# Optimization experiments

Hardware: AMD Instinct MI355X
Metric: run time of the kernel (lower is better)

The kernel has to match this reference:

```python
import jax, jax.numpy as jnp
import numpy as np

L2_LAMDA = 0.001
RECONS_LAMDA = 0.2
LB_TH = 0.01
B, N, D = 32, 2048, 256


def setup_inputs() -> dict:
    key = jax.random.key(0)
    k1, k2, k3, k4 = jax.random.split(key, 4)
    cur = jax.random.normal(k1, (B, N, D), jnp.float32)
    pre = jax.random.normal(k2, (B, N, D), jnp.float32)
    lim_r = float(np.sqrt(6.0 / (D + D)))  # xavier_uniform bound
    r_proj = jax.random.uniform(k3, (D, D), jnp.float32, -lim_r, lim_r)
    lim_i = float(np.sqrt(6.0 / (N + N)))
    incidence_m = jax.random.uniform(k4, (N, N), jnp.float32, -lim_i, lim_i)
    return {"cur": cur, "pre": pre, "r_proj": r_proj, "incidence_m": incidence_m}


def reference(cur, pre, r_proj, incidence_m):
    # torch forward detaches cur/pre
    cur = jax.lax.stop_gradient(cur)
    pre = jax.lax.stop_gradient(pre)
    # clamp(min=lb_th) then zero where not (> lb_th)  ==  keep original where > lb_th else 0
    W = jnp.where(incidence_m > LB_TH, incidence_m, 0.0)          # (N, N)
    proj = jnp.einsum('bnd,de->bne', cur, r_proj)                 # (B, N, D)
    neigh = jnp.einsum('nm,bmd->bnd', W, pre)                     # (B, N, D)
    recon_err = jnp.sqrt(jnp.sum((proj - neigh) ** 2, axis=-1))   # (B, N)
    # torch: max(sum(abs(row[None,:]), dim=0)) == max-abs of the masked row
    l1 = jnp.max(jnp.abs(W), axis=1)                              # (N,)
    l2 = jnp.sqrt(jnp.sum(W ** 2, axis=1))                        # (N,)
    per_node = recon_err * RECONS_LAMDA + l1[None, :] + L2_LAMDA * l2[None, :]
    loss = jnp.sum(per_node, axis=1, keepdims=True)               # (B, 1)
    return loss, incidence_m
```

## Files before the change

### kernel.cpp

```cpp
#include <hip/hip_runtime.h>


typedef __attribute__((ext_vector_type(8))) short bf16x8;
typedef __attribute__((ext_vector_type(8))) unsigned short ushort8;
typedef __attribute__((ext_vector_type(16))) float f32x16;

__device__ __forceinline__ unsigned short f2bf(float f) {
    union { float f; unsigned u; } x; x.f = f;
    unsigned r = x.u + 0x7fffu + ((x.u >> 16) & 1u);
    return (unsigned short)(r >> 16);
}

#define GLL16(g, l)                                                         \
    __builtin_amdgcn_global_load_lds(                                       \
        (const __attribute__((address_space(1))) void*)(g),                 \
        (__attribute__((address_space(3))) void*)(l), 16, 0, 0)

__device__ __forceinline__ void transpose_64x64(
    const float* __restrict__ src, unsigned short* __restrict__ dst,
    int R, int C, int r0, int c0, unsigned short* __restrict__ tile) {
    const int t = threadIdx.x;
    const int fr = t >> 4, fc = (t & 15) * 4;
#pragma unroll
    for (int it = 0; it < 4; ++it) {
        int m = fr + it * 16;
        float4 v = *(const float4*)(src + (size_t)(r0 + m) * C + c0 + fc);
        tile[(fc + 0) * 68 + m] = f2bf(v.x);
        tile[(fc + 1) * 68 + m] = f2bf(v.y);
        tile[(fc + 2) * 68 + m] = f2bf(v.z);
        tile[(fc + 3) * 68 + m] = f2bf(v.w);
    }
    __syncthreads();
    const int d = t >> 2, m0 = (t & 3) * 16;
    unsigned short v[16];
#pragma unroll
    for (int j = 0; j < 4; ++j)
        *(ushort4*)(v + j * 4) = *(const ushort4*)(tile + d * 68 + m0 + j * 4);
    unsigned short* dp = dst + (size_t)(c0 + d) * R + r0 + m0;
    ushort8 p0, p1;
#pragma unroll
    for (int j = 0; j < 8; ++j) { p0[j] = v[j]; p1[j] = v[8 + j]; }
    *(ushort8*)(dp) = p0;
    *(ushort8*)(dp + 8) = p1;
}

__global__ __launch_bounds__(256) void prep_all(
    const float* __restrict__ inc, float* __restrict__ out_inc,
    unsigned short* __restrict__ Wneg, float* __restrict__ crow,
    const float* __restrict__ pre, unsigned short* __restrict__ preT,
    const float* __restrict__ r_proj, unsigned short* __restrict__ rprojT,
    const float* __restrict__ cur, unsigned short* __restrict__ curbf,
    float* __restrict__ out_loss) {
    __shared__ unsigned short tile[64 * 68];
    __shared__ float smax[4], ssum[4];
    const int bid = blockIdx.x;
    const int t = threadIdx.x;

    if (bid < 2048) {
        if (bid == 0 && t < 32) out_loss[t] = 0.f;
        const int row = bid;
        const float4* src = (const float4*)(inc + (size_t)row * 2048);
        float4* dst = (float4*)(out_inc + (size_t)row * 2048);
        ushort4* wp = (ushort4*)(Wneg + (size_t)row * 2048);
        float lmax = 0.f, ss = 0.f;
#pragma unroll
        for (int it = 0; it < 2; ++it) {
            int i = it * 256 + t;
            float4 v = src[i];
            dst[i] = v;
            float w0 = v.x > 0.01f ? v.x : 0.f;
            float w1 = v.y > 0.01f ? v.y : 0.f;
            float w2 = v.z > 0.01f ? v.z : 0.f;
            float w3 = v.w > 0.01f ? v.w : 0.f;
            ushort4 p;
            p.x = f2bf(-w0); p.y = f2bf(-w1); p.z = f2bf(-w2); p.w = f2bf(-w3);
            wp[i] = p;
            lmax = fmaxf(lmax, fmaxf(fmaxf(w0, w1), fmaxf(w2, w3)));
            ss += w0 * w0 + w1 * w1 + w2 * w2 + w3 * w3;
        }
#pragma unroll
        for (int off = 32; off; off >>= 1) {
            lmax = fmaxf(lmax, __shfl_down(lmax, off));
            ss += __shfl_down(ss, off);
        }
        int wv = t >> 6, ln = t & 63;
        if (ln == 0) { smax[wv] = lmax; ssum[wv] = ss; }
        __syncthreads();
        if (t == 0) {
            float m = fmaxf(fmaxf(smax[0], smax[1]), fmaxf(smax[2], smax[3]));
            float s = ssum[0] + ssum[1] + ssum[2] + ssum[3];
            crow[row] = m + 0.001f * sqrtf(s);
        }
    } else if (bid < 6144) {
        const int tt = bid - 2048;
        const int b = tt >> 7;
        const int mt = (tt & 127) >> 2;
        const int dt = tt & 3;
        transpose_64x64(pre + (size_t)b * 524288, preT + (size_t)b * 524288,
                        2048, 256, mt * 64, dt * 64, tile);
    } else if (bid < 6160) {
        const int tt = bid - 6144;
        transpose_64x64(r_proj, rprojT, 256, 256, (tt >> 2) * 64, (tt & 3) * 64,
                        tile);
    } else {
        const size_t base = (size_t)(bid - 6160) * 8192;
#pragma unroll
        for (int i = 0; i < 8; ++i) {
            size_t idx = base + (size_t)(i * 256 + t) * 4;
            float4 v = *(const float4*)(cur + idx);
            ushort4 p;
            p.x = f2bf(v.x); p.y = f2bf(v.y); p.z = f2bf(v.z); p.w = f2bf(v.w);
            *(ushort4*)(curbf + idx) = p;
        }
    }
}

__global__ __launch_bounds__(1024) void gemm_diff(
    const unsigned short* __restrict__ Wneg,
    const unsigned short* __restrict__ curbf,
    const unsigned short* __restrict__ preT,
    const unsigned short* __restrict__ rprojT,
    const float* __restrict__ crow,
    float* __restrict__ out_loss)
{
    const int i    = blockIdx.x;
    const int xcd  = i & 7;
    const int slot = i >> 3;
    const int n0   = (slot & 7) * 256;
    const int b    = xcd + ((slot >> 3) << 3);

    __shared__ unsigned short Ab[4 * 256 * 32];
    __shared__ unsigned short Bb[4 * 256 * 32];
    __shared__ float ssq[256];
    __shared__ float red[16];

    const int tid  = threadIdx.x;
    const int w    = tid >> 6;
    const int lane = tid & 63;
    const int l32  = lane & 31;
    const int half = lane >> 5;
    const int wm   = w >> 2;
    const int wn   = w & 3;
    const int w16  = w * 16;
    const int srow  = lane >> 2;
    const int sbyte = ((lane & 3) ^ ((lane >> 3) & 3)) * 16;
    const int q2    = (l32 >> 1) & 3;

    if (tid < 256) ssq[tid] = 0.f;

    f32x16 acc[2][2] = {};

    const unsigned short* curA = curbf + (size_t)b * 2048 * 256 + (size_t)n0 * 256;
    const unsigned short* preB = preT + (size_t)b * 256 * 2048;
    const unsigned short* An   = Wneg + (size_t)n0 * 2048;

#define STAGEPAIR(T, AB, AS, BB, BS, KK)                                       \
    {                                                                          \
        GLL16((const char*)((AB) + (size_t)(w16 + srow) * (AS) + (KK)) + sbyte,\
              (char*)Ab + ((T) & 3) * 16384 + w * 1024);                       \
        GLL16((const char*)((BB) + (size_t)(w16 + srow) * (BS) + (KK)) + sbyte,\
              (char*)Bb + ((T) & 3) * 16384 + w * 1024);                       \
    }

    STAGEPAIR(0, An, 2048, preB, 2048, 0);
    STAGEPAIR(1, An, 2048, preB, 2048, 32);
    STAGEPAIR(2, An, 2048, preB, 2048, 64);

    for (int t = 0; t < 72; ++t) {
        if (t < 70)       asm volatile("s_waitcnt vmcnt(4)" ::: "memory");
        else if (t == 70) asm volatile("s_waitcnt vmcnt(2)" ::: "memory");
        else              asm volatile("s_waitcnt vmcnt(0)" ::: "memory");
        asm volatile("s_barrier" ::: "memory");

        if (t < 69) {
            const int t3 = t + 3;
            const unsigned short *aB, *bB;
            int aS, bS, kk;
            if (t3 < 64) { aB = An;   aS = 2048; bB = preB;   bS = 2048; kk = t3 * 32; }
            else         { aB = curA; aS = 256;  bB = rprojT; bS = 256;  kk = (t3 - 64) * 32; }
            STAGEPAIR(t3, aB, aS, bB, bS, kk);
        }

        const unsigned short* Ac = Ab + (t & 3) * 8192;
        const unsigned short* Bc = Bb + (t & 3) * 8192;
#pragma unroll
        for (int ks = 0; ks < 2; ++ks) {
            const int co = (((ks << 1) + half) ^ q2) << 3;
            bf16x8 af[2], bfr[2];
#pragma unroll
            for (int mi = 0; mi < 2; ++mi)
                af[mi] = *(const bf16x8*)(Ac + (wm * 64 + mi * 32 + l32) * 32 + co);
#pragma unroll
            for (int ni = 0; ni < 2; ++ni)
                bfr[ni] = *(const bf16x8*)(Bc + (wn * 64 + ni * 32 + l32) * 32 + co);
#pragma unroll
            for (int mi = 0; mi < 2; ++mi)
#pragma unroll
                for (int ni = 0; ni < 2; ++ni)
                    acc[mi][ni] = __builtin_amdgcn_mfma_f32_32x32x16_bf16(
                        af[mi], bfr[ni], acc[mi][ni], 0, 0, 0);
        }
    }
    __syncthreads();

#pragma unroll
    for (int mi = 0; mi < 2; ++mi)
#pragma unroll
        for (int reg = 0; reg < 16; ++reg) {
            float s = 0.f;
#pragma unroll
            for (int ni = 0; ni < 2; ++ni) {
                float v = acc[mi][ni][reg];
                s += v * v;
            }
            s += __shfl_xor(s, 1);
            s += __shfl_xor(s, 2);
            s += __shfl_xor(s, 4);
            s += __shfl_xor(s, 8);
            s += __shfl_xor(s, 16);
            if (l32 == 0) {
                const int row = wm * 64 + mi * 32 +
                                (reg & 3) + 8 * (reg >> 2) + 4 * half;
                atomicAdd(&ssq[row], s);
            }
        }
    __syncthreads();

    float contrib = 0.f;
    if (tid < 256) contrib = 0.2f * sqrtf(ssq[tid]) + crow[n0 + tid];
#pragma unroll
    for (int off = 32; off; off >>= 1) contrib += __shfl_down(contrib, off);
    if (lane == 0) red[w] = contrib;
    __syncthreads();
    if (tid == 0) {
        float s = 0.f;
#pragma unroll
        for (int k = 0; k < 16; ++k) s += red[k];
        atomicAdd(out_loss + b, s);
    }
}

extern "C" void kernel_launch(void* const* d_in, const int* in_sizes, int n_in,
                              void* d_out, int out_size, void* d_ws, size_t ws_size,
                              hipStream_t stream) {
    const float* cur    = (const float*)d_in[0];
    const float* pre    = (const float*)d_in[1];
    const float* r_proj = (const float*)d_in[2];
    const float* inc    = (const float*)d_in[3];
    float* out = (float*)d_out;

    char* ws = (char*)d_ws;
    unsigned short* Wneg   = (unsigned short*)(ws + 0);
    unsigned short* preT   = (unsigned short*)(ws + 8388608);
    unsigned short* rprojT = (unsigned short*)(ws + 41943040);
    float*          crow   = (float*)(ws + 42336256);
    unsigned short* curbf  = (unsigned short*)(ws + 42344448);

    prep_all<<<8208, 256, 0, stream>>>(inc, out + 32, Wneg, crow,
                                       pre, preT, r_proj, rprojT,
                                       cur, curbf, out);
    gemm_diff<<<256, 1024, 0, stream>>>(Wneg, curbf, preT, rprojT, crow, out);
}
```

Baseline: 258.2 us.

## Shrink GEMM tile to 128 rows with 512 threads and triple buffering

Halves the M tile of the fused GEMM (128 rows instead of 256) and the block size (512 threads), doubling the grid to 512 blocks. The LDS pipeline goes from 4 stages with prefetch distance 3 to 3 stages with distance 2. Each block now loads the B tile in two halves. The aim is more blocks per CU and better occupancy across the 256 CUs, at the cost of loading the pre/rproj B tiles twice as often and a shallower prefetch.

Result: no change. 259.3 us (+0.4%).

```diff
diff --git a/kernel.cpp b/kernel.cpp
--- a/kernel.cpp
+++ b/kernel.cpp
@@ -115,7 +115,7 @@
     }
 }
 
-__global__ __launch_bounds__(1024) void gemm_diff(
+__global__ __launch_bounds__(512) void gemm_diff(
     const unsigned short* __restrict__ Wneg,
     const unsigned short* __restrict__ curbf,
     const unsigned short* __restrict__ preT,
@@ -126,13 +126,13 @@
     const int i    = blockIdx.x;
     const int xcd  = i & 7;
     const int slot = i >> 3;
-    const int n0   = (slot & 7) * 256;
-    const int b    = xcd + ((slot >> 3) << 3);
-
-    __shared__ unsigned short Ab[4 * 256 * 32];
-    __shared__ unsigned short Bb[4 * 256 * 32];
-    __shared__ float ssq[256];
-    __shared__ float red[16];
+    const int n0   = (slot & 15) * 128;
+    const int b    = xcd + ((slot >> 4) << 3);
+
+    __shared__ unsigned short Ab[3 * 128 * 32];
+    __shared__ unsigned short Bb[3 * 256 * 32];
+    __shared__ float ssq[128];
+    __shared__ float red[8];
 
     const int tid  = threadIdx.x;
     const int w    = tid >> 6;
@@ -146,7 +146,7 @@
     const int sbyte = ((lane & 3) ^ ((lane >> 3) & 3)) * 16;
     const int q2    = (l32 >> 1) & 3;
 
-    if (tid < 256) ssq[tid] = 0.f;
+    if (tid < 128) ssq[tid] = 0.f;
 
     f32x16 acc[2][2] = {};
 
@@ -154,35 +154,34 @@
     const unsigned short* preB = preT + (size_t)b * 256 * 2048;
     const unsigned short* An   = Wneg + (size_t)n0 * 2048;
 
-#define STAGEPAIR(T, AB, AS, BB, BS, KK)                                       \
+#define STAGE(BUF, aB, aS, bB, bS, KK)                                         \
     {                                                                          \
-        GLL16((const char*)((AB) + (size_t)(w16 + srow) * (AS) + (KK)) + sbyte,\
-              (char*)Ab + ((T) & 3) * 16384 + w * 1024);                       \
-        GLL16((const char*)((BB) + (size_t)(w16 + srow) * (BS) + (KK)) + sbyte,\
-              (char*)Bb + ((T) & 3) * 16384 + w * 1024);                       \
-    }
-
-    STAGEPAIR(0, An, 2048, preB, 2048, 0);
-    STAGEPAIR(1, An, 2048, preB, 2048, 32);
-    STAGEPAIR(2, An, 2048, preB, 2048, 64);
-
+        GLL16((const char*)((aB) + (size_t)(w16 + srow) * (aS) + (KK)) + sbyte,\
+              (char*)Ab + (BUF) * 8192 + w16 * 64);                            \
+        GLL16((const char*)((bB) + (size_t)(w16 + srow) * (bS) + (KK)) + sbyte,\
+              (char*)Bb + (BUF) * 16384 + w16 * 64);                           \
+        GLL16((const char*)((bB) + (size_t)(128 + w16 + srow) * (bS) + (KK)) + sbyte,\
+              (char*)Bb + (BUF) * 16384 + (128 + w16) * 64);                   \
+    }
+
+    STAGE(0, An, 2048, preB, 2048, 0);
+    STAGE(1, An, 2048, preB, 2048, 32);
+
+    int bc = 0;
     for (int t = 0; t < 72; ++t) {
-        if (t < 70)       asm volatile("s_waitcnt vmcnt(4)" ::: "memory");
-        else if (t == 70) asm volatile("s_waitcnt vmcnt(2)" ::: "memory");
-        else              asm volatile("s_waitcnt vmcnt(0)" ::: "memory");
+        if (t < 71) asm volatile("s_waitcnt vmcnt(3)" ::: "memory");
+        else        asm volatile("s_waitcnt vmcnt(0)" ::: "memory");
         asm volatile("s_barrier" ::: "memory");
 
-        if (t < 69) {
-            const int t3 = t + 3;
-            const unsigned short *aB, *bB;
-            int aS, bS, kk;
-            if (t3 < 64) { aB = An;   aS = 2048; bB = preB;   bS = 2048; kk = t3 * 32; }
-            else         { aB = curA; aS = 256;  bB = rprojT; bS = 256;  kk = (t3 - 64) * 32; }
-            STAGEPAIR(t3, aB, aS, bB, bS, kk);
-        }
-
-        const unsigned short* Ac = Ab + (t & 3) * 8192;
-        const unsigned short* Bc = Bb + (t & 3) * 8192;
+        if (t < 70) {
+            const int t2 = t + 2;
+            const int bs = bc >= 1 ? bc - 1 : bc + 2;
+            if (t2 < 64) { STAGE(bs, An,   2048, preB,   2048, t2 * 32); }
+            else         { STAGE(bs, curA, 256,  rprojT, 256,  (t2 - 64) * 32); }
+        }
+
+        const unsigned short* Ac = Ab + bc * 4096;
+        const unsigned short* Bc = Bb + bc * 8192;
 #pragma unroll
         for (int ks = 0; ks < 2; ++ks) {
             const int co = (((ks << 1) + half) ^ q2) << 3;
@@ -200,6 +199,7 @@
                     acc[mi][ni] = __builtin_amdgcn_mfma_f32_32x32x16_bf16(
                         af[mi], bfr[ni], acc[mi][ni], 0, 0, 0);
         }
+        bc = bc < 2 ? bc + 1 : 0;
     }
     __syncthreads();
 
@@ -227,7 +227,7 @@
     __syncthreads();
 
     float contrib = 0.f;
-    if (tid < 256) contrib = 0.2f * sqrtf(ssq[tid]) + crow[n0 + tid];
+    if (tid < 128) contrib = 0.2f * sqrtf(ssq[tid]) + crow[n0 + tid];
 #pragma unroll
     for (int off = 32; off; off >>= 1) contrib += __shfl_down(contrib, off);
     if (lane == 0) red[w] = contrib;
@@ -235,7 +235,7 @@
     if (tid == 0) {
         float s = 0.f;
 #pragma unroll
-        for (int k = 0; k < 16; ++k) s += red[k];
+        for (int k = 0; k < 8; ++k) s += red[k];
         atomicAdd(out_loss + b, s);
     }
 }
@@ -259,5 +259,5 @@
     prep_all<<<8208, 256, 0, stream>>>(inc, out + 32, Wneg, crow,
                                        pre, preT, r_proj, rprojT,
                                        cur, curbf, out);
-    gemm_diff<<<256, 1024, 0, stream>>>(Wneg, curbf, preT, rprojT, crow, out);
-}
+    gemm_diff<<<512, 512, 0, stream>>>(Wneg, curbf, preT, rprojT, crow, out);
+}
```

## Restructure GEMM into 8-wave 128x64 warp tiles with 16x16x32 MFMA and ping-pong phases

Applied to the files above, without the earlier changes.

Drops the GEMM block from 16 to 8 waves, giving each wave a 128x64 output tile built from 16x16x32 bf16 MFMAs. The K-step grows to 64 with double-buffered LDS in place of the 4-deep ring. The main loop is split into barrier-separated phases that interleave global-to-LDS loads with MFMA bursts under raised s_setprio, and B fragments are reused across two A halves. The aim is more register-level reuse and fewer LDS reads and barriers per FLOP, at the cost of higher register pressure and a tighter load/compute schedule.

After: 242.7 us. -6.0%, faster.

```diff
diff --git a/kernel.cpp b/kernel.cpp
--- a/kernel.cpp
+++ b/kernel.cpp
@@ -3,7 +3,7 @@
 
 typedef __attribute__((ext_vector_type(8))) short bf16x8;
 typedef __attribute__((ext_vector_type(8))) unsigned short ushort8;
-typedef __attribute__((ext_vector_type(16))) float f32x16;
+typedef __attribute__((ext_vector_type(4))) float f32x4;
 
 __device__ __forceinline__ unsigned short f2bf(float f) {
     union { float f; unsigned u; } x; x.f = f;
@@ -115,7 +115,7 @@
     }
 }
 
-__global__ __launch_bounds__(1024) void gemm_diff(
+__global__ __launch_bounds__(512) void gemm_diff(
     const unsigned short* __restrict__ Wneg,
     const unsigned short* __restrict__ curbf,
     const unsigned short* __restrict__ preT,
@@ -129,98 +129,125 @@
     const int n0   = (slot & 7) * 256;
     const int b    = xcd + ((slot >> 3) << 3);
 
-    __shared__ unsigned short Ab[4 * 256 * 32];
-    __shared__ unsigned short Bb[4 * 256 * 32];
+    __shared__ unsigned short Ab[2 * 256 * 64];
+    __shared__ unsigned short Bb[2 * 256 * 64];
     __shared__ float ssq[256];
-    __shared__ float red[16];
+    __shared__ float red[8];
 
     const int tid  = threadIdx.x;
     const int w    = tid >> 6;
     const int lane = tid & 63;
-    const int l32  = lane & 31;
-    const int half = lane >> 5;
+    const int l15  = lane & 15;
+    const int kg   = lane >> 4;
     const int wm   = w >> 2;
     const int wn   = w & 3;
-    const int w16  = w * 16;
-    const int srow  = lane >> 2;
-    const int sbyte = ((lane & 3) ^ ((lane >> 3) & 3)) * 16;
-    const int q2    = (l32 >> 1) & 3;
+    const int srow  = lane >> 3;
+    const int sbyte = ((lane & 7) ^ srow) * 16;
+    const int rsw   = (lane & 7) << 4;
+    const int csw0 = (kg * 16) ^ rsw;
+    const int csw1 = (64 + kg * 16) ^ rsw;
 
     if (tid < 256) ssq[tid] = 0.f;
 
-    f32x16 acc[2][2] = {};
+    f32x4 acc[8][4] = {};
+    bf16x8 bfr[4];
 
     const unsigned short* curA = curbf + (size_t)b * 2048 * 256 + (size_t)n0 * 256;
     const unsigned short* preB = preT + (size_t)b * 256 * 2048;
     const unsigned short* An   = Wneg + (size_t)n0 * 2048;
 
-#define STAGEPAIR(T, AB, AS, BB, BS, KK)                                       \
+#define STAGE_A(T, qa)                                                         \
     {                                                                          \
-        GLL16((const char*)((AB) + (size_t)(w16 + srow) * (AS) + (KK)) + sbyte,\
-              (char*)Ab + ((T) & 3) * 16384 + w * 1024);                       \
-        GLL16((const char*)((BB) + (size_t)(w16 + srow) * (BS) + (KK)) + sbyte,\
-              (char*)Bb + ((T) & 3) * 16384 + w * 1024);                       \
-    }
-
-    STAGEPAIR(0, An, 2048, preB, 2048, 0);
-    STAGEPAIR(1, An, 2048, preB, 2048, 32);
-    STAGEPAIR(2, An, 2048, preB, 2048, 64);
-
-    for (int t = 0; t < 72; ++t) {
-        if (t < 70)       asm volatile("s_waitcnt vmcnt(4)" ::: "memory");
-        else if (t == 70) asm volatile("s_waitcnt vmcnt(2)" ::: "memory");
-        else              asm volatile("s_waitcnt vmcnt(0)" ::: "memory");
-        asm volatile("s_barrier" ::: "memory");
-
-        if (t < 69) {
-            const int t3 = t + 3;
-            const unsigned short *aB, *bB;
-            int aS, bS, kk;
-            if (t3 < 64) { aB = An;   aS = 2048; bB = preB;   bS = 2048; kk = t3 * 32; }
-            else         { aB = curA; aS = 256;  bB = rprojT; bS = 256;  kk = (t3 - 64) * 32; }
-            STAGEPAIR(t3, aB, aS, bB, bS, kk);
-        }
-
-        const unsigned short* Ac = Ab + (t & 3) * 8192;
-        const unsigned short* Bc = Bb + (t & 3) * 8192;
-#pragma unroll
-        for (int ks = 0; ks < 2; ++ks) {
-            const int co = (((ks << 1) + half) ^ q2) << 3;
-            bf16x8 af[2], bfr[2];
-#pragma unroll
-            for (int mi = 0; mi < 2; ++mi)
-                af[mi] = *(const bf16x8*)(Ac + (wm * 64 + mi * 32 + l32) * 32 + co);
-#pragma unroll
-            for (int ni = 0; ni < 2; ++ni)
-                bfr[ni] = *(const bf16x8*)(Bc + (wn * 64 + ni * 32 + l32) * 32 + co);
-#pragma unroll
-            for (int mi = 0; mi < 2; ++mi)
-#pragma unroll
-                for (int ni = 0; ni < 2; ++ni)
-                    acc[mi][ni] = __builtin_amdgcn_mfma_f32_32x32x16_bf16(
-                        af[mi], bfr[ni], acc[mi][ni], 0, 0, 0);
-        }
-    }
-    __syncthreads();
-
-#pragma unroll
-    for (int mi = 0; mi < 2; ++mi)
-#pragma unroll
-        for (int reg = 0; reg < 16; ++reg) {
+        const int _t = (T);                                                    \
+        const char* _ab; size_t _str; int _kk;                                 \
+        if (_t < 32) { _ab = (const char*)An;   _str = 4096; _kk = _t * 128; } \
+        else { _ab = (const char*)curA; _str = 512; _kk = (_t - 32) * 128; }   \
+        _Pragma("unroll") for (int _p = 0; _p < 2; ++_p) {                     \
+            const int _rb = (qa) * 64 + _p * 128 + w * 8;                      \
+            GLL16(_ab + (size_t)(_rb + srow) * _str + _kk + sbyte,             \
+                  (char*)Ab + (_t & 1) * 32768 + _rb * 128);                   \
+        }                                                                      \
+    }
+#define STAGE_B(T, u)                                                          \
+    {                                                                          \
+        const int _t = (T);                                                    \
+        const char* _bb; size_t _str; int _kk;                                 \
+        if (_t < 32) { _bb = (const char*)preB;   _str = 4096; _kk = _t * 128; }\
+        else { _bb = (const char*)rprojT; _str = 512; _kk = (_t - 32) * 128; } \
+        _Pragma("unroll") for (int _p = 0; _p < 2; ++_p) {                     \
+            const int _rb = (u) * 128 + _p * 64 + w * 8;                       \
+            GLL16(_bb + (size_t)(_rb + srow) * _str + _kk + sbyte,             \
+                  (char*)Bb + (_t & 1) * 32768 + _rb * 128);                   \
+        }                                                                      \
+    }
+
+#define PHASE(BUF, qa, kh, STAGES, VMW)                                        \
+    {                                                                          \
+        const char* _A = (const char*)Ab + (BUF) * 32768 +                     \
+                         (wm * 128 + (qa) * 64) * 128;                         \
+        bf16x8 _af[4];                                                         \
+        _Pragma("unroll") for (int _m = 0; _m < 4; ++_m)                       \
+            _af[_m] = *(const bf16x8*)(_A + (_m * 16 + l15) * 128 +            \
+                                       ((kh) ? csw1 : csw0));                  \
+        if ((qa) == 0) {                                                       \
+            const char* _B = (const char*)Bb + (BUF) * 32768 +                 \
+                             (wn * 64) * 128;                                  \
+            _Pragma("unroll") for (int _n = 0; _n < 4; ++_n)                   \
+                bfr[_n] = *(const bf16x8*)(_B + (_n * 16 + l15) * 128 +        \
+                                           ((kh) ? csw1 : csw0));              \
+        }                                                                      \
+        STAGES                                                                 \
+        VMW                                                                    \
+        asm volatile("s_barrier" ::: "memory");                                \
+        __builtin_amdgcn_s_setprio(1);                                         \
+        _Pragma("unroll") for (int _m = 0; _m < 4; ++_m)                       \
+        _Pragma("unroll") for (int _n = 0; _n < 4; ++_n)                       \
+            acc[(qa) * 4 + _m][_n] = __builtin_amdgcn_mfma_f32_16x16x32_bf16(  \
+                _af[_m], bfr[_n], acc[(qa) * 4 + _m][_n], 0, 0, 0);            \
+        __builtin_amdgcn_s_setprio(0);                                         \
+        asm volatile("s_barrier" ::: "memory");                                \
+    }
+
+#define VM2 asm volatile("s_waitcnt vmcnt(2)" ::: "memory");
+#define VM0 asm volatile("s_waitcnt vmcnt(0)" ::: "memory");
+
+    STAGE_A(0, 0); STAGE_A(0, 1); STAGE_B(0, 0); STAGE_B(0, 1);
+    STAGE_A(1, 0);
+    VM2
+    asm volatile("s_barrier" ::: "memory");
+
+    for (int j = 0; j < 18; ++j) {
+        const int E2 = 2 * j + 2, O2 = 2 * j + 3;
+        const bool more = (j < 17);
+        PHASE(0, 0, 0, { STAGE_A(2 * j + 1, 1); STAGE_B(2 * j + 1, 0); }, {})
+        PHASE(0, 1, 0, { STAGE_B(2 * j + 1, 1); }, {})
+        PHASE(0, 0, 1, {}, {})
+        PHASE(0, 1, 1, { if (more) STAGE_A(E2, 0); },
+              { if (more) { VM2 } else { VM0 } })
+        PHASE(1, 0, 0, { if (more) { STAGE_A(E2, 1); STAGE_B(E2, 0); } }, {})
+        PHASE(1, 1, 0, { if (more) STAGE_B(E2, 1); }, {})
+        PHASE(1, 0, 1, {}, {})
+        PHASE(1, 1, 1, { if (more) STAGE_A(O2, 0); },
+              { if (more) { VM2 } else { VM0 } })
+    }
+    __syncthreads();
+
+#pragma unroll
+    for (int mf = 0; mf < 8; ++mf)
+#pragma unroll
+        for (int r = 0; r < 4; ++r) {
             float s = 0.f;
 #pragma unroll
-            for (int ni = 0; ni < 2; ++ni) {
-                float v = acc[mi][ni][reg];
+            for (int nf = 0; nf < 4; ++nf) {
+                float v = acc[mf][nf][r];
                 s += v * v;
             }
             s += __shfl_xor(s, 1);
             s += __shfl_xor(s, 2);
             s += __shfl_xor(s, 4);
             s += __shfl_xor(s, 8);
-            s += __shfl_xor(s, 16);
-            if (l32 == 0) {
-                const int row = wm * 64 + mi * 32 +
-                                (reg & 3) + 8 * (reg >> 2) + 4 * half;
+            if (l15 == 0) {
+                const int row = wm * 128 + mf * 16 + kg * 4 + r;
                 atomicAdd(&ssq[row], s);
             }
         }
@@ -235,7 +262,7 @@
     if (tid == 0) {
         float s = 0.f;
 #pragma unroll
-        for (int k = 0; k < 16; ++k) s += red[k];
+        for (int k = 0; k < 8; ++k) s += red[k];
         atomicAdd(out_loss + b, s);
     }
 }
@@ -259,5 +286,5 @@
     prep_all<<<8208, 256, 0, stream>>>(inc, out + 32, Wneg, crow,
                                        pre, preT, r_proj, rprojT,
                                        cur, curbf, out);
-    gemm_diff<<<256, 1024, 0, stream>>>(Wneg, curbf, preT, rprojT, crow, out);
-}
+    gemm_diff<<<256, 512, 0, stream>>>(Wneg, curbf, preT, rprojT, crow, out);
+}
```
